# Kernel tuning notes

Hardware: AMD Instinct MI355X
Metric: run time of the kernel (lower is better)

## Reference

```python
import jax, jax.numpy as jnp
import numpy as np

N = 100000
E = 1600000
D_IN = 64
D_OUT = 64


def setup_inputs() -> dict:
    key = jax.random.key(0)
    k1, k2, k3, k4, k5 = jax.random.split(key, 5)
    x = jax.random.normal(k1, (N, D_IN), dtype=jnp.float32)
    edge_index = jax.random.randint(k2, (2, E), 0, N, dtype=jnp.int64)
    edge_attr = jax.random.uniform(k3, (E,), dtype=jnp.float32)
    # GraphConv params: lin_rel (with bias) applied to aggregated messages,
    # lin_root (no bias) applied to root/self features.
    scale = 1.0 / np.sqrt(D_IN)
    W_rel = jax.random.uniform(k4, (D_OUT, D_IN), dtype=jnp.float32, minval=-scale, maxval=scale)
    b_rel = jnp.zeros((D_OUT,), dtype=jnp.float32)
    W_root = jax.random.uniform(k5, (D_OUT, D_IN), dtype=jnp.float32, minval=-scale, maxval=scale)
    return {"x": x, "edge_index": edge_index, "edge_attr": edge_attr,
            "W_rel": W_rel, "b_rel": b_rel, "W_root": W_root}


def reference(x, edge_index, edge_attr, W_rel, b_rel, W_root):
    src = edge_index[0]  # message sources (x_j)
    dst = edge_index[1]  # message targets (aggregation index)
    # message: x_j * edge_weight, then sum-aggregate at target nodes
    msgs = x[src] * edge_attr[:, None]                     # [E, D_IN]
    agg = jax.ops.segment_sum(msgs, dst, num_segments=N)   # [N, D_IN]
    # GraphConv: lin_rel(agg) + lin_root(x)
    out = agg @ W_rel.T + b_rel + x @ W_root.T             # [N, D_OUT]
    return jax.nn.relu(out)
```

## Files before the change

kernel.cpp:

```cpp
#include <hip/hip_runtime.h>
#include <hip/hip_bf16.h>

#define N_NODES 100000
#define N_EDGES 1600000
#define D 64
#define SLOT 48
#define WSCALE 32767.0f

#define BSHIFT 8
#define BNODES 256
#define NB 391
#define CAP_B 4672
#define CHUNK 4096
#define NBIN_BLOCKS ((N_EDGES + CHUNK - 1) / CHUNK)

#define BPT 512
#define EPT (CHUNK / BPT)
#define PREP_BLOCKS (N_NODES * D / 4 / BPT)
#define FUSED_GRID (NBIN_BLOCKS + PREP_BLOCKS + 1)

__device__ inline ushort f2bu(float f) {
    __hip_bfloat16 h = __float2bfloat16(f);
    return *(ushort*)&h;
}

__global__ __launch_bounds__(BPT) void bin_prep_kernel(
    const int* __restrict__ src,
    const int* __restrict__ dst,
    const float* __restrict__ w,
    int* __restrict__ gcur,
    int2* __restrict__ bucketed,
    const float* __restrict__ x,
    ushort* __restrict__ xb,
    const float* __restrict__ Wrel,
    const float* __restrict__ Wroot,
    ushort* __restrict__ wb)
{
    __shared__ int h[NB];
    __shared__ int sc[BPT];
    __shared__ int cur[NB];
    __shared__ int gbase[NB];
    __shared__ int2 sbuf[CHUNK];
    int tid = threadIdx.x;

    if (blockIdx.x >= NBIN_BLOCKS) {
        int pb = blockIdx.x - NBIN_BLOCKS;
        if (pb == PREP_BLOCKS) {
            for (int i = tid; i < 2 * D * D; i += BPT) {
                float f = (i < D * D) ? Wrel[i] : Wroot[i - D * D];
                wb[i] = f2bu(f);
            }
        } else {
            int i = (pb * BPT + tid) * 4;
            float4 v = *(const float4*)(x + i);
            ushort4 o;
            o.x = f2bu(v.x); o.y = f2bu(v.y); o.z = f2bu(v.z); o.w = f2bu(v.w);
            *(ushort4*)(xb + i) = o;
        }
        return;
    }

    for (int b = tid; b < NB; b += BPT) h[b] = 0;
    __syncthreads();

    int e0 = blockIdx.x * CHUNK;
    int d[EPT], pk[EPT];
#pragma unroll
    for (int k = 0; k < EPT; ++k) {
        int e  = e0 + k * BPT + tid;
        int ec = min(e, N_EDGES - 1);
        int dd = dst[ec];
        int q  = (int)(w[ec] * WSCALE + 0.5f);
        q = min(q, 32767);
        pk[k] = src[ec] | (q << 17);
        d[k]  = (e < N_EDGES) ? dd : -1;
        if (d[k] >= 0) atomicAdd(&h[dd >> BSHIFT], 1);
    }
    __syncthreads();

    sc[tid] = (tid < NB) ? h[tid] : 0;
    __syncthreads();
#pragma unroll
    for (int off = 1; off < BPT; off <<= 1) {
        int v = sc[tid];
        int u = (tid >= off) ? sc[tid - off] : 0;
        __syncthreads();
        sc[tid] = v + u;
        __syncthreads();
    }

    if (tid < NB) {
        int c = h[tid];
        gbase[tid] = (c > 0) ? atomicAdd(&gcur[tid], c) : 0;
        cur[tid]   = (tid > 0) ? sc[tid - 1] : 0;
    }
    __syncthreads();

#pragma unroll
    for (int k = 0; k < EPT; ++k) {
        if (d[k] >= 0) {
            int b = d[k] >> BSHIFT;
            int p = atomicAdd(&cur[b], 1);
            sbuf[p] = make_int2(pk[k], d[k]);
        }
    }
    __syncthreads();

    int total = sc[NB - 1];
    for (int i = tid; i < total; i += BPT) {
        int2 v   = sbuf[i];
        int dd   = v.y;
        int b    = dd >> BSHIFT;
        int excl = (b > 0) ? sc[b - 1] : 0;
        int gpos = gbase[b] + (i - excl);
        if (gpos < CAP_B)
            bucketed[(size_t)b * CAP_B + gpos] = make_int2(v.x, dd & (BNODES - 1));
    }
}

#define FG_T 1024

__global__ __launch_bounds__(FG_T) void fill_gather_kernel(
    const int* __restrict__ gcur,
    const int2* __restrict__ bucketed,
    const ushort* __restrict__ xb,
    ushort* __restrict__ aggb)
{
    __shared__ int lcnt[BNODES];
    __shared__ unsigned __align__(16) img[BNODES * SLOT];
    int tid = threadIdx.x;
    int b   = blockIdx.x;

    for (int i = tid; i < BNODES; i += FG_T) lcnt[i] = 0;
    __syncthreads();

    int nE = min(gcur[b], CAP_B);
    const int2* __restrict__ be = bucketed + (size_t)b * CAP_B;
    for (int i = tid; i < nE; i += FG_T) {
        int2 v = be[i];
        int p = atomicAdd(&lcnt[v.y], 1);
        if (p < SLOT)
            img[v.y * SLOT + p] = (unsigned)v.x;
    }
    __syncthreads();

    int g = tid >> 3;
    int t = tid & 7;

    for (int n = g; n < BNODES; n += 128) {
        int node = b * BNODES + n;
        if (node >= N_NODES) break;
        int dg = min(lcnt[n], SLOT);
        const unsigned* __restrict__ row = &img[n * SLOT];

        float a0 = 0.f, a1 = 0.f, a2 = 0.f, a3 = 0.f;
        float a4 = 0.f, a5 = 0.f, a6 = 0.f, a7 = 0.f;
#pragma unroll 2
        for (int j = 0; j < dg; ++j) {
            unsigned v = row[j];
            int s = v & 0x1FFFF;
            float wv = (float)(v >> 17) * (1.0f / WSCALE);
            uint4 dx = *(const uint4*)(xb + (size_t)s * D + 8 * t);
            a0 += __uint_as_float(dx.x << 16)         * wv;
            a1 += __uint_as_float(dx.x & 0xFFFF0000u) * wv;
            a2 += __uint_as_float(dx.y << 16)         * wv;
            a3 += __uint_as_float(dx.y & 0xFFFF0000u) * wv;
            a4 += __uint_as_float(dx.z << 16)         * wv;
            a5 += __uint_as_float(dx.z & 0xFFFF0000u) * wv;
            a6 += __uint_as_float(dx.w << 16)         * wv;
            a7 += __uint_as_float(dx.w & 0xFFFF0000u) * wv;
        }

        union { ushort u[8]; uint4 q; } pk;
        pk.u[0] = f2bu(a0); pk.u[1] = f2bu(a1);
        pk.u[2] = f2bu(a2); pk.u[3] = f2bu(a3);
        pk.u[4] = f2bu(a4); pk.u[5] = f2bu(a5);
        pk.u[6] = f2bu(a6); pk.u[7] = f2bu(a7);
        *(uint4*)(aggb + (size_t)node * D + 8 * t) = pk.q;
    }
}

typedef __attribute__((ext_vector_type(8))) short bf8;
typedef __attribute__((ext_vector_type(4))) float f4;

__global__ __launch_bounds__(256) void linear_kernel(
    const ushort* __restrict__ xb,
    const ushort* __restrict__ aggb,
    float* __restrict__ out,
    const ushort* __restrict__ wb,
    const float* __restrict__ brel)
{
    __shared__ float __align__(16) sOut[4][16][68];

    int tid  = threadIdx.x;
    int wv   = tid >> 6, lane = tid & 63;
    int node0 = (blockIdx.x * 4 + wv) * 16;
    if (node0 >= N_NODES) return;

    int m    = lane & 15;
    int quad = lane >> 4;

    bf8 bw[2][4][2];
#pragma unroll
    for (int mat = 0; mat < 2; ++mat)
#pragma unroll
        for (int nt = 0; nt < 4; ++nt)
#pragma unroll
            for (int s = 0; s < 2; ++s)
                bw[mat][nt][s] = *(const bf8*)(wb + mat * D * D
                                               + (16 * nt + m) * 64 + s * 32 + quad * 8);

    const ushort* ar = aggb + (size_t)(node0 + m) * 64 + quad * 8;
    bf8 aagg0 = *(const bf8*)ar;
    bf8 aagg1 = *(const bf8*)(ar + 32);
    const ushort* xr = xb + (size_t)(node0 + m) * 64 + quad * 8;
    bf8 ax0 = *(const bf8*)xr;
    bf8 ax1 = *(const bf8*)(xr + 32);

    f4 acc[4];
#pragma unroll
    for (int nt = 0; nt < 4; ++nt) {
        float b = brel[16 * nt + m];
        f4 c = {b, b, b, b};
        c = __builtin_amdgcn_mfma_f32_16x16x32_bf16(aagg0, bw[0][nt][0], c, 0, 0, 0);
        c = __builtin_amdgcn_mfma_f32_16x16x32_bf16(aagg1, bw[0][nt][1], c, 0, 0, 0);
        c = __builtin_amdgcn_mfma_f32_16x16x32_bf16(ax0,   bw[1][nt][0], c, 0, 0, 0);
        c = __builtin_amdgcn_mfma_f32_16x16x32_bf16(ax1,   bw[1][nt][1], c, 0, 0, 0);
        acc[nt] = c;
    }

#pragma unroll
    for (int nt = 0; nt < 4; ++nt)
#pragma unroll
        for (int r = 0; r < 4; ++r)
            sOut[wv][quad * 4 + r][16 * nt + m] = fmaxf(acc[nt][r], 0.f);
#pragma unroll
    for (int p = 0; p < 4; ++p) {
        int idx = p * 64 + lane;
        int row = idx >> 4;
        int c4  = (idx & 15) * 4;
        float4 v = *(const float4*)&sOut[wv][row][c4];
        *(float4*)(out + (size_t)(node0 + row) * 64 + c4) = v;
    }
}

extern "C" void kernel_launch(void* const* d_in, const int* in_sizes, int n_in,
                              void* d_out, int out_size, void* d_ws, size_t ws_size,
                              hipStream_t stream)
{
    const float* x     = (const float*)d_in[0];
    const int*   eidx  = (const int*)d_in[1];
    const float* eattr = (const float*)d_in[2];
    const float* Wrel  = (const float*)d_in[3];
    const float* brel  = (const float*)d_in[4];
    const float* Wroot = (const float*)d_in[5];
    float* out = (float*)d_out;

    const int* src = eidx;
    const int* dst = eidx + N_EDGES;

    int*      gcur     = (int*)d_ws;
    int2*     bucketed = (int2*)(gcur + 1024);
    ushort*   xb       = (ushort*)(bucketed + (size_t)NB * CAP_B);
    ushort*   wb       = xb + (size_t)N_NODES * D;
    ushort*   aggb     = wb + 2 * D * D;

    hipMemsetAsync(gcur, 0, NB * sizeof(int), stream);

    bin_prep_kernel<<<FUSED_GRID, BPT, 0, stream>>>(src, dst, eattr, gcur, bucketed,
                                                    x, xb, Wrel, Wroot, wb);
    fill_gather_kernel<<<NB, FG_T, 0, stream>>>(gcur, bucketed, xb, aggb);
    linear_kernel<<<(N_NODES + 63) / 64, 256, 0, stream>>>(xb, aggb, out, wb, brel);
}
```

Before: 157.5 us.

## Fuse the linear/MFMA stage into the gather kernel's epilogue

Removes the separate linear kernel launch. After each block finishes aggregating its 256-node bucket, it syncs and its 16 waves each run the bf16 MFMA transform on 16 nodes, reading back the just-written aggregates and writing ReLU output directly. This saves a kernel launch and lets the linear work reuse cache-resident data. In exchange, the output stores become scalar per lane instead of LDS-staged float4 stores. Register pressure in a 1024-thread block may also rise.

```diff
diff --git a/kernel.cpp b/kernel.cpp
--- a/kernel.cpp
+++ b/kernel.cpp
@@ -120,11 +120,17 @@
 
 #define FG_T 1024
 
-__global__ __launch_bounds__(FG_T) void fill_gather_kernel(
+typedef __attribute__((ext_vector_type(8))) short bf8;
+typedef __attribute__((ext_vector_type(4))) float f4;
+
+__global__ __launch_bounds__(FG_T) void fgl_kernel(
     const int* __restrict__ gcur,
     const int2* __restrict__ bucketed,
     const ushort* __restrict__ xb,
-    ushort* __restrict__ aggb)
+    ushort* __restrict__ aggb,
+    const ushort* __restrict__ wb,
+    const float* __restrict__ brel,
+    float* __restrict__ out)
 {
     __shared__ int lcnt[BNODES];
     __shared__ unsigned __align__(16) img[BNODES * SLOT];
@@ -178,69 +184,39 @@
         pk.u[6] = f2bu(a6); pk.u[7] = f2bu(a7);
         *(uint4*)(aggb + (size_t)node * D + 8 * t) = pk.q;
     }
-}
-
-typedef __attribute__((ext_vector_type(8))) short bf8;
-typedef __attribute__((ext_vector_type(4))) float f4;
-
-__global__ __launch_bounds__(256) void linear_kernel(
-    const ushort* __restrict__ xb,
-    const ushort* __restrict__ aggb,
-    float* __restrict__ out,
-    const ushort* __restrict__ wb,
-    const float* __restrict__ brel)
-{
-    __shared__ float __align__(16) sOut[4][16][68];
-
-    int tid  = threadIdx.x;
+    __syncthreads();
+
     int wv   = tid >> 6, lane = tid & 63;
-    int node0 = (blockIdx.x * 4 + wv) * 16;
+    int node0 = b * BNODES + wv * 16;
     if (node0 >= N_NODES) return;
 
     int m    = lane & 15;
     int quad = lane >> 4;
 
-    bf8 bw[2][4][2];
-#pragma unroll
-    for (int mat = 0; mat < 2; ++mat)
-#pragma unroll
-        for (int nt = 0; nt < 4; ++nt)
-#pragma unroll
-            for (int s = 0; s < 2; ++s)
-                bw[mat][nt][s] = *(const bf8*)(wb + mat * D * D
-                                               + (16 * nt + m) * 64 + s * 32 + quad * 8);
-
-    const ushort* ar = aggb + (size_t)(node0 + m) * 64 + quad * 8;
+    const ushort* ar = aggb + (size_t)(node0 + m) * D + quad * 8;
     bf8 aagg0 = *(const bf8*)ar;
     bf8 aagg1 = *(const bf8*)(ar + 32);
-    const ushort* xr = xb + (size_t)(node0 + m) * 64 + quad * 8;
+    const ushort* xr = xb + (size_t)(node0 + m) * D + quad * 8;
     bf8 ax0 = *(const bf8*)xr;
     bf8 ax1 = *(const bf8*)(xr + 32);
 
-    f4 acc[4];
 #pragma unroll
     for (int nt = 0; nt < 4; ++nt) {
-        float b = brel[16 * nt + m];
-        f4 c = {b, b, b, b};
-        c = __builtin_amdgcn_mfma_f32_16x16x32_bf16(aagg0, bw[0][nt][0], c, 0, 0, 0);
-        c = __builtin_amdgcn_mfma_f32_16x16x32_bf16(aagg1, bw[0][nt][1], c, 0, 0, 0);
-        c = __builtin_amdgcn_mfma_f32_16x16x32_bf16(ax0,   bw[1][nt][0], c, 0, 0, 0);
-        c = __builtin_amdgcn_mfma_f32_16x16x32_bf16(ax1,   bw[1][nt][1], c, 0, 0, 0);
-        acc[nt] = c;
-    }
-
-#pragma unroll
-    for (int nt = 0; nt < 4; ++nt)
+        const ushort* wr = wb + (16 * nt + m) * D + quad * 8;
+        bf8 b00 = *(const bf8*)(wr);
+        bf8 b01 = *(const bf8*)(wr + 32);
+        bf8 b10 = *(const bf8*)(wr + D * D);
+        bf8 b11 = *(const bf8*)(wr + D * D + 32);
+        float bb = brel[16 * nt + m];
+        f4 c = {bb, bb, bb, bb};
+        c = __builtin_amdgcn_mfma_f32_16x16x32_bf16(aagg0, b00, c, 0, 0, 0);
+        c = __builtin_amdgcn_mfma_f32_16x16x32_bf16(aagg1, b01, c, 0, 0, 0);
+        c = __builtin_amdgcn_mfma_f32_16x16x32_bf16(ax0,   b10, c, 0, 0, 0);
+        c = __builtin_amdgcn_mfma_f32_16x16x32_bf16(ax1,   b11, c, 0, 0, 0);
 #pragma unroll
         for (int r = 0; r < 4; ++r)
-            sOut[wv][quad * 4 + r][16 * nt + m] = fmaxf(acc[nt][r], 0.f);
-#pragma unroll
-    for (int p = 0; p < 4; ++p) {
-        int idx = p * 64 + lane;
-        int row = idx >> 4;
-        int c4  = (idx & 15) * 4;
-        float4 v = *(const float4*)&sOut[wv][row][c4];
-        *(float4*)(out + (size_t)(node0 + row) * 64 + c4) = v;
+            out[(size_t)(node0 + quad * 4 + r) * D + 16 * nt + m] =
+                fmaxf(c[r], 0.f);
     }
 }
 
@@ -269,6 +245,5 @@
 
     bin_prep_kernel<<<FUSED_GRID, BPT, 0, stream>>>(src, dst, eattr, gcur, bucketed,
                                                     x, xb, Wrel, Wroot, wb);
-    fill_gather_kernel<<<NB, FG_T, 0, stream>>>(gcur, bucketed, xb, aggb);
-    linear_kernel<<<(N_NODES + 63) / 64, 256, 0, stream>>>(xb, aggb, out, wb, brel);
-}
+    fgl_kernel<<<NB, FG_T, 0, stream>>>(gcur, bucketed, xb, aggb, wb, brel, out);
+}
```

After: 154.8 us. Within noise of the previous version (-1.7%).
